# Optimization experiments

Hardware: AMD Instinct MI355X
Metric: run time of the kernel (lower is better)

Reference implementation:

```python
import jax, jax.numpy as jnp
import numpy as np

N_EMB = 1024
N_HEADS = 16
HS = N_EMB // N_HEADS  # 64
BASE = 10000.0


def _rope_cache(T):
    # theta uses dim = n_emb (as in the source), sliced to hs//2 frequencies
    i = jnp.arange(HS // 2, dtype=jnp.float32)
    theta = BASE ** (-2.0 * i / N_EMB)            # [hs/2]
    pos = jnp.arange(T, dtype=jnp.float32)        # [T]
    ang = pos[:, None] * theta[None, :]           # [T, hs/2]
    return jnp.cos(ang), jnp.sin(ang)


def _apply_rope(x, cos, sin):
    # x: [B, T, nh, hs]; rotate consecutive pairs along hs
    b, t, nh, hs = x.shape
    xr = x.reshape(b, t, nh, hs // 2, 2)
    c = cos[None, :, None, :]
    s = sin[None, :, None, :]
    r0 = xr[..., 0] * c - xr[..., 1] * s
    r1 = xr[..., 1] * c + xr[..., 0] * s
    return jnp.stack([r0, r1], axis=-1).reshape(b, t, nh, hs)


def setup_inputs() -> dict:
    key = jax.random.key(0)
    k1, k2, k3, k4 = jax.random.split(key, 4)
    B, T = 2, 2048
    w_std = 0.02
    x = jax.random.normal(k1, (B, T, N_EMB), jnp.float32)
    Wq = jax.random.normal(k2, (N_EMB, N_EMB), jnp.float32) * w_std
    Wk = jax.random.normal(k3, (N_EMB, N_EMB), jnp.float32) * w_std
    Wv = jax.random.normal(k4, (N_EMB, N_EMB), jnp.float32) * w_std
    return {"x": x, "Wq": Wq, "Wk": Wk, "Wv": Wv}


def reference(x, Wq, Wk, Wv):
    B, T, C = x.shape
    # nn.Linear(bias=False): y = x @ W.T
    q = (x @ Wq.T).reshape(B, T, N_HEADS, HS)
    k = (x @ Wk.T).reshape(B, T, N_HEADS, HS)
    v = (x @ Wv.T).reshape(B, T, N_HEADS, HS)
    cos, sin = _rope_cache(T)
    q = _apply_rope(q, cos, sin)
    k = _apply_rope(k, cos, sin)
    # scale uses C (n_emb), as in the source (not head_size)
    wei = jnp.einsum('bqhd,bkhd->bhqk', q, k) * (C ** -0.5)  # [B, nh, T, T]
    mask = jnp.tril(jnp.ones((T, T), dtype=bool))
    wei = jnp.where(mask[None, None], wei, -jnp.inf)
    wei = jax.nn.softmax(wei, axis=-1)
    # dropout is identity in eval mode
    out = jnp.einsum('bhqk,bkhd->bqhd', wei, v).reshape(B, T, C)
    return out
```

## Files before the change

kernel.cpp:

```cpp
#include <hip/hip_runtime.h>
#include <stdint.h>

typedef unsigned short u16;
typedef __bf16 bf16x8 __attribute__((ext_vector_type(8)));
typedef unsigned short u16x8 __attribute__((ext_vector_type(8)));
typedef float f32x4 __attribute__((ext_vector_type(4)));
typedef uint32_t u32v4 __attribute__((ext_vector_type(4)));

#define LOG2E 1.4426950408889634f

typedef const __attribute__((address_space(1))) uint32_t as1_u32;
typedef __attribute__((address_space(3))) uint32_t as3_u32;

__device__ __forceinline__ u16 f2bf(float f) {
  union { float f; uint32_t i; } v; v.f = f;
  uint32_t r = (v.i + 0x7fffu + ((v.i >> 16) & 1u)) >> 16;
  return (u16)r;
}
__device__ __forceinline__ float bf2f(u16 u) {
  union { uint32_t i; float f; } v; v.i = ((uint32_t)u) << 16; return v.f;
}

__device__ __forceinline__ void gld_lds16(const void* g, void* l) {
  as1_u32* gp = (as1_u32*)((uintptr_t)g);
  as3_u32* lp = (as3_u32*)(uint32_t)(uintptr_t)(l);
  __builtin_amdgcn_global_load_lds(gp, lp, 16, 0, 0);
}

__device__ __forceinline__ float fast_exp2(float x) {
  float r;
  asm("v_exp_f32 %0, %1" : "=v"(r) : "v"(x));
  return r;
}

__global__ __launch_bounds__(256) void f32_to_bf16(
    const float* __restrict__ x, const float* __restrict__ wq,
    const float* __restrict__ wk, const float* __restrict__ wv,
    u16* __restrict__ xc, u16* __restrict__ wqc,
    u16* __restrict__ wkc, u16* __restrict__ wvc) {
  const int z = blockIdx.y;
  const float* src = z == 0 ? x : (z == 1 ? wq : (z == 2 ? wk : wv));
  u16* dst = z == 0 ? xc : (z == 1 ? wqc : (z == 2 ? wkc : wvc));
  const int n = z == 0 ? (1 << 22) : (1 << 20);

  const int idx = (blockIdx.x * 256 + (int)threadIdx.x) * 8;
  if (idx >= n) return;
  const f32x4 a = *(const f32x4*)&src[idx];
  const f32x4 b = *(const f32x4*)&src[idx + 4];
  u16x8 o;
#pragma unroll
  for (int j = 0; j < 4; j++) { o[j] = f2bf(a[j]); o[j + 4] = f2bf(b[j]); }
  *(u16x8*)&dst[idx] = o;
}

__global__ __launch_bounds__(256) void qkv_gemm(
    const u16* __restrict__ xc, const u16* __restrict__ wqc,
    const u16* __restrict__ wkc, const u16* __restrict__ wvc,
    u16* __restrict__ qo, u16* __restrict__ ko, u16* __restrict__ vt) {
  __shared__ __align__(16) u16 As[128 * 64];
  __shared__ __align__(16) u16 Bs[128 * 64];

  const int tid = threadIdx.x;
  const int lane = tid & 63;
  const int w = tid >> 6;
  const int wm = w >> 1, wn = w & 1;
  const int quad = lane >> 4, m16 = lane & 15;

  const int id    = (int)blockIdx.x;
  const int xcd   = id & 7;
  const int local = id >> 3;
  const int by    = xcd * 4 + (local & 3);
  const int rest  = local >> 2;
  const int which = rest % 3;
  const int bx    = rest / 3;

  const u16* __restrict__ Ap;
  const u16* __restrict__ Bp;
  int m0, n0;
  if (which == 2) {
    Ap = wvc; Bp = xc;
    m0 = bx * 128;
    n0 = by * 128;
  } else {
    Ap = xc; Bp = which == 0 ? wqc : wkc;
    m0 = by * 128;
    n0 = bx * 128;
  }

  const f32x4 z4 = {0.f, 0.f, 0.f, 0.f};
  f32x4 acc[4][4];
#pragma unroll
  for (int i = 0; i < 4; i++)
#pragma unroll
    for (int j = 0; j < 4; j++) acc[i][j] = z4;

  const int lrow = lane >> 3;
  const int scol = ((lane & 7) ^ (lrow & 7)) * 8;
  const int srowA = m0 + w * 32 + lrow;
  const int srowB = n0 + w * 32 + lrow;
  const int rsw = m16 & 7;

  for (int k0 = 0; k0 < 1024; k0 += 64) {
    __syncthreads();
#pragma unroll
    for (int j = 0; j < 4; j++) {
      gld_lds16(&Ap[(size_t)(srowA + j * 8) * 1024 + k0 + scol],
                &As[(w * 32 + j * 8) * 64]);
      gld_lds16(&Bp[(size_t)(srowB + j * 8) * 1024 + k0 + scol],
                &Bs[(w * 32 + j * 8) * 64]);
    }
    __syncthreads();

#pragma unroll
    for (int kk = 0; kk < 2; kk++) {
      bf16x8 af[4], bfr[4];
#pragma unroll
      for (int t = 0; t < 4; t++) {
        af[t] = *(const bf16x8*)
            &As[(wm * 64 + t * 16 + m16) * 64 + (((kk * 4 + quad) ^ rsw) * 8)];
        bfr[t] = *(const bf16x8*)
            &Bs[(wn * 64 + t * 16 + m16) * 64 + (((kk * 4 + quad) ^ rsw) * 8)];
      }
#pragma unroll
      for (int mt = 0; mt < 4; mt++)
#pragma unroll
        for (int nt = 0; nt < 4; nt++)
          acc[mt][nt] = __builtin_amdgcn_mfma_f32_16x16x32_bf16(
              af[mt], bfr[nt], acc[mt][nt], 0, 0, 0);
    }
  }

  if (which < 2) {
    u16* __restrict__ out = which == 0 ? qo : ko;
#pragma unroll
    for (int mt = 0; mt < 4; mt++) {
      const int row = m0 + wm * 64 + mt * 16 + quad * 4;
#pragma unroll
      for (int nt = 0; nt < 4; nt++) {
        const int n = n0 + wn * 64 + nt * 16 + m16;
        f32x4 a = acc[mt][nt];
#pragma unroll
        for (int r = 0; r < 4; r++)
          out[(size_t)(row + r) * 1024 + n] = f2bf(a[r]);
      }
    }
  } else {
    const int m16p = (m16 & 3) | ((m16 & 4) << 1) | ((m16 & 8) >> 1);
#pragma unroll
    for (int mt = 0; mt < 4; mt++) {
      const int row = m0 + wm * 64 + mt * 16 + quad * 4;
#pragma unroll
      for (int nt = 0; nt < 4; nt++) {
        const int n = n0 + wn * 64 + nt * 16 + m16p;
        f32x4 a = acc[mt][nt];
#pragma unroll
        for (int r = 0; r < 4; r++)
          vt[(size_t)(row + r) * 4096 + n] = f2bf(a[r]);
      }
    }
  }
}

__global__ __launch_bounds__(256) void rope_inplace(u16* __restrict__ qb,
                                                    u16* __restrict__ kb) {
  u16* buf = blockIdx.y == 0 ? qb : kb;
  const int p = blockIdx.x * 256 + (int)threadIdx.x;
  const int e0 = p * 8;
  const int row = e0 >> 10;
  const int col0 = e0 & 1023;
  const int t = row & 2047;
  const float tf = (float)t;

  u16x8 d = *(const u16x8*)&buf[(size_t)row * 1024 + col0];
  u16x8 o;
#pragma unroll
  for (int j = 0; j < 4; j++) {
    const int i = ((col0 & 63) >> 1) + j;
    const float th = fast_exp2(-(float)i * 0.02595256324130752f);
    const float rev = tf * th * 0.15915494309189535f;
    float fr, s, c;
    asm("v_fract_f32 %0, %1" : "=v"(fr) : "v"(rev));
    asm("v_sin_f32 %0, %1" : "=v"(s) : "v"(fr));
    asm("v_cos_f32 %0, %1" : "=v"(c) : "v"(fr));
    const float a0 = bf2f(d[2 * j]), a1 = bf2f(d[2 * j + 1]);
    o[2 * j]     = f2bf(a0 * c - a1 * s);
    o[2 * j + 1] = f2bf(a1 * c + a0 * s);
  }
  *(u16x8*)&buf[(size_t)row * 1024 + col0] = o;
}

__global__ __launch_bounds__(256, 2) void flash_attn(
    const u16* __restrict__ qg, const u16* __restrict__ kg,
    const u16* __restrict__ vt, float* __restrict__ out) {
  __shared__ __align__(16) u16 Ks[2][128 * 72];
  __shared__ __align__(16) u16 Vs[2][64 * 136];

  const int tid = threadIdx.x, lane = tid & 63, w = tid >> 6;
  const int quad = lane >> 4, m16 = lane & 15;

  const int id    = (int)blockIdx.x;
  const int lower = id & 255;
  const int j     = id >> 8;
  const int X     = lower & 7;
  const int vloc  = (lower >> 3) & 3;
  const int kk_   = lower >> 5;
  const int Q     = j ? 15 - kk_ : kk_;
  const int v     = X * 4 + vloc;
  const int h     = v & 15;
  const int b     = v >> 4;

  const size_t base  = (size_t)b * 2048 * 1024 + (size_t)h * 64;
  const size_t vbase = (size_t)(h * 64) * 4096 + (size_t)b * 2048;
  const float SC = 0.03125f * LOG2E;
  const f32x4 z4 = {0.f, 0.f, 0.f, 0.f};
  const int srow = tid >> 2, sc = (tid & 3) * 16;

  union { u16x8 u; bf16x8 f; } ones;
#pragma unroll
  for (int k = 0; k < 8; k++) ones.u[k] = 0x3F80;

  const int q0 = Q * 128;
  const int nr = Q + 1;

  const u16* qsA = &qg[base + (size_t)(q0 + w * 32 + m16) * 1024 + quad * 8];
  const bf16x8 qfA0 = *(const bf16x8*)qsA;
  const bf16x8 qfA1 = *(const bf16x8*)(qsA + 32);
  const u16* qsB = qsA + (size_t)16 * 1024;
  const bf16x8 qfB0 = *(const bf16x8*)qsB;
  const bf16x8 qfB1 = *(const bf16x8*)(qsB + 32);

  u16x8 kr0, kr1, kr2, kr3, vr0, vr1, vr2, vr3;
  {
    const u16* ks = &kg[base + (size_t)srow * 1024 + sc];
    kr0 = *(const u16x8*)ks; kr1 = *(const u16x8*)(ks + 8);
    const u16* ks2 = ks + (size_t)64 * 1024;
    kr2 = *(const u16x8*)ks2; kr3 = *(const u16x8*)(ks2 + 8);
    const u16* vs = &vt[vbase + (size_t)srow * 4096 + sc];
    vr0 = *(const u16x8*)vs; vr1 = *(const u16x8*)(vs + 8);
    vr2 = *(const u16x8*)(vs + 64); vr3 = *(const u16x8*)(vs + 72);
  }

  f32x4 lA = z4, lB = z4;
  f32x4 OA[4], OB[4];
#pragma unroll
  for (int d = 0; d < 4; d++) { OA[d] = z4; OB[d] = z4; }

  const int qrowA = q0 + w * 32 + quad * 4;
  const int qcolA = q0 + w * 32 + m16;

  int p = 0;
  for (int rr = 0; rr < nr; ++rr) {
    const int k0 = rr * 128;
    u16* ksp = &Ks[p][0];
    u16* vsp = &Vs[p][0];
    *(u16x8*)&ksp[srow * 72 + sc] = kr0;
    *(u16x8*)&ksp[srow * 72 + sc + 8] = kr1;
    *(u16x8*)&ksp[(64 + srow) * 72 + sc] = kr2;
    *(u16x8*)&ksp[(64 + srow) * 72 + sc + 8] = kr3;
    *(u16x8*)&vsp[srow * 136 + sc] = vr0;
    *(u16x8*)&vsp[srow * 136 + sc + 8] = vr1;
    *(u16x8*)&vsp[srow * 136 + 64 + sc] = vr2;
    *(u16x8*)&vsp[srow * 136 + 64 + sc + 8] = vr3;
    if (rr + 1 < nr) {
      const u16* ks = &kg[base + (size_t)(k0 + 128 + srow) * 1024 + sc];
      kr0 = *(const u16x8*)ks; kr1 = *(const u16x8*)(ks + 8);
      const u16* ks2 = ks + (size_t)64 * 1024;
      kr2 = *(const u16x8*)ks2; kr3 = *(const u16x8*)(ks2 + 8);
      const u16* vs = &vt[vbase + (size_t)srow * 4096 + k0 + 128 + sc];
      vr0 = *(const u16x8*)vs; vr1 = *(const u16x8*)(vs + 8);
      vr2 = *(const u16x8*)(vs + 64); vr3 = *(const u16x8*)(vs + 72);
    }
    __syncthreads();

    f32x4 SA[8], SB[8];
#pragma unroll
    for (int nt = 0; nt < 8; nt++) {
      const bf16x8 kf0 = *(const bf16x8*)&ksp[(nt * 16 + m16) * 72 + quad * 8];
      const bf16x8 kf1 =
          *(const bf16x8*)&ksp[(nt * 16 + m16) * 72 + 32 + quad * 8];
      SA[nt] = __builtin_amdgcn_mfma_f32_16x16x32_bf16(kf0, qfA0, z4, 0, 0, 0);
      SA[nt] = __builtin_amdgcn_mfma_f32_16x16x32_bf16(kf1, qfA1, SA[nt], 0, 0, 0);
      SB[nt] = __builtin_amdgcn_mfma_f32_16x16x32_bf16(kf0, qfB0, z4, 0, 0, 0);
      SB[nt] = __builtin_amdgcn_mfma_f32_16x16x32_bf16(kf1, qfB1, SB[nt], 0, 0, 0);
    }

    const bool lastr = (rr == nr - 1);

    union { u32v4 u; bf16x8 f; } PA[4], PB[4];
    {
      uint32_t W[16];
#pragma unroll
      for (int nt = 0; nt < 8; nt++) {
        float pe[4];
#pragma unroll
        for (int r = 0; r < 4; r++) {
          float e = fast_exp2(SA[nt][r] * SC);
          const int key = k0 + nt * 16 + quad * 4 + r;
          if (lastr && key > qcolA) e = 0.f;
          pe[r] = e;
        }
        uint32_t w0, w1;
        asm("v_cvt_pk_bf16_f32 %0, %1, %2" : "=v"(w0) : "v"(pe[0]), "v"(pe[1]));
        asm("v_cvt_pk_bf16_f32 %0, %1, %2" : "=v"(w1) : "v"(pe[2]), "v"(pe[3]));
        W[2 * nt] = w0; W[2 * nt + 1] = w1;
      }
#pragma unroll
      for (int ks = 0; ks < 4; ks++) {
        uint32_t a0 = W[4 * ks], b0 = W[4 * ks + 2];
        uint32_t a1 = W[4 * ks + 1], b1 = W[4 * ks + 3];
        asm("v_permlane32_swap_b32 %0, %1" : "+v"(a0), "+v"(b0));
        asm("v_permlane32_swap_b32 %0, %1" : "+v"(a1), "+v"(b1));
        PA[ks].u = (u32v4){a0, a1, b0, b1};
      }
    }
    {
      const int qcolB = qcolA + 16;
      uint32_t W[16];
#pragma unroll
      for (int nt = 0; nt < 8; nt++) {
        float pe[4];
#pragma unroll
        for (int r = 0; r < 4; r++) {
          float e = fast_exp2(SB[nt][r] * SC);
          const int key = k0 + nt * 16 + quad * 4 + r;
          if (lastr && key > qcolB) e = 0.f;
          pe[r] = e;
        }
        uint32_t w0, w1;
        asm("v_cvt_pk_bf16_f32 %0, %1, %2" : "=v"(w0) : "v"(pe[0]), "v"(pe[1]));
        asm("v_cvt_pk_bf16_f32 %0, %1, %2" : "=v"(w1) : "v"(pe[2]), "v"(pe[3]));
        W[2 * nt] = w0; W[2 * nt + 1] = w1;
      }
#pragma unroll
      for (int ks = 0; ks < 4; ks++) {
        uint32_t a0 = W[4 * ks], b0 = W[4 * ks + 2];
        uint32_t a1 = W[4 * ks + 1], b1 = W[4 * ks + 3];
        asm("v_permlane32_swap_b32 %0, %1" : "+v"(a0), "+v"(b0));
        asm("v_permlane32_swap_b32 %0, %1" : "+v"(a1), "+v"(b1));
        PB[ks].u = (u32v4){a0, a1, b0, b1};
      }
    }

#pragma unroll
    for (int ks = 0; ks < 4; ks++) {
      lA = __builtin_amdgcn_mfma_f32_16x16x32_bf16(PA[ks].f, ones.f, lA, 0, 0, 0);
      lB = __builtin_amdgcn_mfma_f32_16x16x32_bf16(PB[ks].f, ones.f, lB, 0, 0, 0);
    }

#pragma unroll
    for (int dt = 0; dt < 4; dt++) {
#pragma unroll
      for (int ks = 0; ks < 4; ks++) {
        const bf16x8 vf =
            *(const bf16x8*)&vsp[(dt * 16 + m16) * 136 + ks * 32 + quad * 8];
        OA[dt] = __builtin_amdgcn_mfma_f32_16x16x32_bf16(PA[ks].f, vf, OA[dt],
                                                         0, 0, 0);
        OB[dt] = __builtin_amdgcn_mfma_f32_16x16x32_bf16(PB[ks].f, vf, OB[dt],
                                                         0, 0, 0);
      }
    }
    p ^= 1;
  }

  float invA[4], invB[4];
#pragma unroll
  for (int r = 0; r < 4; r++) { invA[r] = 1.0f / lA[r]; invB[r] = 1.0f / lB[r]; }

#pragma unroll
  for (int dt = 0; dt < 4; dt++)
#pragma unroll
    for (int r = 0; r < 4; r++) {
      out[base + (size_t)(qrowA + r) * 1024 + dt * 16 + m16] =
          OA[dt][r] * invA[r];
      out[base + (size_t)(qrowA + 16 + r) * 1024 + dt * 16 + m16] =
          OB[dt][r] * invB[r];
    }
}

extern "C" void kernel_launch(void* const* d_in, const int* in_sizes, int n_in,
                              void* d_out, int out_size, void* d_ws, size_t ws_size,
                              hipStream_t stream) {
  const float* x  = (const float*)d_in[0];
  const float* Wq = (const float*)d_in[1];
  const float* Wk = (const float*)d_in[2];
  const float* Wv = (const float*)d_in[3];
  u16* qb  = (u16*)d_ws;
  u16* kb  = qb  + (size_t)4096 * 1024;
  u16* vtw = kb  + (size_t)4096 * 1024;
  u16* xc  = vtw + (size_t)4096 * 1024;
  u16* wqc = xc  + (size_t)4096 * 1024;
  u16* wkc = wqc + (size_t)1024 * 1024;
  u16* wvc = wkc + (size_t)1024 * 1024;

  f32_to_bf16<<<dim3(2048, 4), 256, 0, stream>>>(x, Wq, Wk, Wv,
                                                 xc, wqc, wkc, wvc);
  qkv_gemm<<<dim3(768, 1, 1), 256, 0, stream>>>(xc, wqc, wkc, wvc,
                                                qb, kb, vtw);
  rope_inplace<<<dim3(2048, 2), 256, 0, stream>>>(qb, kb);
  flash_attn<<<dim3(512, 1, 1), 256, 0, stream>>>(qb, kb, vtw, (float*)d_out);
}
```

Measured before the change: 152.7 us.

## Load V fragments directly from global memory instead of staging through LDS

Removes the shared-memory V tile and its register prefetch. Each wave now loads its V^T MFMA operands straight from global memory into registers, issued mid-iteration so they overlap the softmax of the B half. The barrier moves to right after the K tile store, ahead of the next K prefetch. This cuts LDS traffic and footprint but makes every wave fetch V independently from global/L2, with 16 extra live bf16x8 registers and latency exposed inside the loop.

```diff
diff --git a/kernel.cpp b/kernel.cpp
--- a/kernel.cpp
+++ b/kernel.cpp
@@ -193,7 +193,6 @@
     const u16* __restrict__ qg, const u16* __restrict__ kg,
     const u16* __restrict__ vt, float* __restrict__ out) {
   __shared__ __align__(16) u16 Ks[2][128 * 72];
-  __shared__ __align__(16) u16 Vs[2][64 * 136];
 
   const int tid = threadIdx.x, lane = tid & 63, w = tid >> 6;
   const int quad = lane >> 4, m16 = lane & 15;
@@ -229,15 +228,12 @@
   const bf16x8 qfB0 = *(const bf16x8*)qsB;
   const bf16x8 qfB1 = *(const bf16x8*)(qsB + 32);
 
-  u16x8 kr0, kr1, kr2, kr3, vr0, vr1, vr2, vr3;
+  u16x8 kr0, kr1, kr2, kr3;
   {
-    const u16* ks = &kg[base + (size_t)srow * 1024 + sc];
-    kr0 = *(const u16x8*)ks; kr1 = *(const u16x8*)(ks + 8);
-    const u16* ks2 = ks + (size_t)64 * 1024;
-    kr2 = *(const u16x8*)ks2; kr3 = *(const u16x8*)(ks2 + 8);
-    const u16* vs = &vt[vbase + (size_t)srow * 4096 + sc];
-    vr0 = *(const u16x8*)vs; vr1 = *(const u16x8*)(vs + 8);
-    vr2 = *(const u16x8*)(vs + 64); vr3 = *(const u16x8*)(vs + 72);
+    const u16* kp = &kg[base + (size_t)srow * 1024 + sc];
+    kr0 = *(const u16x8*)kp; kr1 = *(const u16x8*)(kp + 8);
+    const u16* kp2 = kp + (size_t)64 * 1024;
+    kr2 = *(const u16x8*)kp2; kr3 = *(const u16x8*)(kp2 + 8);
   }
 
   f32x4 lA = z4, lB = z4;
@@ -252,25 +248,18 @@
   for (int rr = 0; rr < nr; ++rr) {
     const int k0 = rr * 128;
     u16* ksp = &Ks[p][0];
-    u16* vsp = &Vs[p][0];
     *(u16x8*)&ksp[srow * 72 + sc] = kr0;
     *(u16x8*)&ksp[srow * 72 + sc + 8] = kr1;
     *(u16x8*)&ksp[(64 + srow) * 72 + sc] = kr2;
     *(u16x8*)&ksp[(64 + srow) * 72 + sc + 8] = kr3;
-    *(u16x8*)&vsp[srow * 136 + sc] = vr0;
-    *(u16x8*)&vsp[srow * 136 + sc + 8] = vr1;
-    *(u16x8*)&vsp[srow * 136 + 64 + sc] = vr2;
-    *(u16x8*)&vsp[srow * 136 + 64 + sc + 8] = vr3;
+    __syncthreads();
+
     if (rr + 1 < nr) {
-      const u16* ks = &kg[base + (size_t)(k0 + 128 + srow) * 1024 + sc];
-      kr0 = *(const u16x8*)ks; kr1 = *(const u16x8*)(ks + 8);
-      const u16* ks2 = ks + (size_t)64 * 1024;
-      kr2 = *(const u16x8*)ks2; kr3 = *(const u16x8*)(ks2 + 8);
-      const u16* vs = &vt[vbase + (size_t)srow * 4096 + k0 + 128 + sc];
-      vr0 = *(const u16x8*)vs; vr1 = *(const u16x8*)(vs + 8);
-      vr2 = *(const u16x8*)(vs + 64); vr3 = *(const u16x8*)(vs + 72);
-    }
-    __syncthreads();
+      const u16* kp = &kg[base + (size_t)(k0 + 128 + srow) * 1024 + sc];
+      kr0 = *(const u16x8*)kp; kr1 = *(const u16x8*)(kp + 8);
+      const u16* kp2 = kp + (size_t)64 * 1024;
+      kr2 = *(const u16x8*)kp2; kr3 = *(const u16x8*)(kp2 + 8);
+    }
 
     f32x4 SA[8], SB[8];
 #pragma unroll
@@ -313,6 +302,15 @@
         PA[ks].u = (u32v4){a0, a1, b0, b1};
       }
     }
+
+    bf16x8 vf[4][4];
+#pragma unroll
+    for (int dt = 0; dt < 4; dt++)
+#pragma unroll
+      for (int ks = 0; ks < 4; ks++)
+        vf[dt][ks] = *(const bf16x8*)
+            &vt[vbase + (size_t)(dt * 16 + m16) * 4096 + k0 + ks * 32 + quad * 8];
+
     {
       const int qcolB = qcolA + 16;
       uint32_t W[16];
@@ -351,12 +349,10 @@
     for (int dt = 0; dt < 4; dt++) {
 #pragma unroll
       for (int ks = 0; ks < 4; ks++) {
-        const bf16x8 vf =
-            *(const bf16x8*)&vsp[(dt * 16 + m16) * 136 + ks * 32 + quad * 8];
-        OA[dt] = __builtin_amdgcn_mfma_f32_16x16x32_bf16(PA[ks].f, vf, OA[dt],
-                                                         0, 0, 0);
-        OB[dt] = __builtin_amdgcn_mfma_f32_16x16x32_bf16(PB[ks].f, vf, OB[dt],
-                                                         0, 0, 0);
+        OA[dt] = __builtin_amdgcn_mfma_f32_16x16x32_bf16(PA[ks].f, vf[dt][ks],
+                                                         OA[dt], 0, 0, 0);
+        OB[dt] = __builtin_amdgcn_mfma_f32_16x16x32_bf16(PB[ks].f, vf[dt][ks],
+                                                         OB[dt], 0, 0, 0);
       }
     }
     p ^= 1;
```

New measurement: 173.1 us. 13.4% more time.

## Triple-buffer QKV GEMM LDS tiles with async prefetch two stages ahead

Applied to the files above, without the earlier changes.

Replaces the single-buffered 64-wide K loop in the QKV projection GEMM with a three-stage ring of 32-wide LDS tiles, so each iteration issues direct global-to-LDS loads two k-steps ahead. Explicit vmcnt/lgkmcnt waits and a single barrier per step stand in for the double __syncthreads. The swizzle is adapted to the narrower tile. This is meant to hide global load latency behind MFMA work, at the cost of more barriers (32 vs 16 k-steps) and fragile hand-tuned wait counts.

```diff
diff --git a/kernel.cpp b/kernel.cpp
--- a/kernel.cpp
+++ b/kernel.cpp
@@ -57,8 +57,8 @@
     const u16* __restrict__ xc, const u16* __restrict__ wqc,
     const u16* __restrict__ wkc, const u16* __restrict__ wvc,
     u16* __restrict__ qo, u16* __restrict__ ko, u16* __restrict__ vt) {
-  __shared__ __align__(16) u16 As[128 * 64];
-  __shared__ __align__(16) u16 Bs[128 * 64];
+  __shared__ __align__(16) u16 As[3][128 * 32];
+  __shared__ __align__(16) u16 Bs[3][128 * 32];
 
   const int tid = threadIdx.x;
   const int lane = tid & 63;
@@ -94,41 +94,51 @@
 #pragma unroll
     for (int j = 0; j < 4; j++) acc[i][j] = z4;
 
-  const int lrow = lane >> 3;
-  const int scol = ((lane & 7) ^ (lrow & 7)) * 8;
+  const int lrow = lane >> 2;
+  const int scol = ((lane & 3) ^ ((lane >> 3) & 3)) * 8;
   const int srowA = m0 + w * 32 + lrow;
   const int srowB = n0 + w * 32 + lrow;
-  const int rsw = m16 & 7;
-
-  for (int k0 = 0; k0 < 1024; k0 += 64) {
-    __syncthreads();
-#pragma unroll
-    for (int j = 0; j < 4; j++) {
-      gld_lds16(&Ap[(size_t)(srowA + j * 8) * 1024 + k0 + scol],
-                &As[(w * 32 + j * 8) * 64]);
-      gld_lds16(&Bp[(size_t)(srowB + j * 8) * 1024 + k0 + scol],
-                &Bs[(w * 32 + j * 8) * 64]);
-    }
-    __syncthreads();
-
-#pragma unroll
-    for (int kk = 0; kk < 2; kk++) {
-      bf16x8 af[4], bfr[4];
-#pragma unroll
-      for (int t = 0; t < 4; t++) {
-        af[t] = *(const bf16x8*)
-            &As[(wm * 64 + t * 16 + m16) * 64 + (((kk * 4 + quad) ^ rsw) * 8)];
-        bfr[t] = *(const bf16x8*)
-            &Bs[(wn * 64 + t * 16 + m16) * 64 + (((kk * 4 + quad) ^ rsw) * 8)];
-      }
-#pragma unroll
-      for (int mt = 0; mt < 4; mt++)
-#pragma unroll
-        for (int nt = 0; nt < 4; nt++)
-          acc[mt][nt] = __builtin_amdgcn_mfma_f32_16x16x32_bf16(
-              af[mt], bfr[nt], acc[mt][nt], 0, 0, 0);
-    }
-  }
+  const int rchunk = (quad ^ ((m16 >> 1) & 3)) * 8;
+
+#define QKV_STAGE(T, B)                                                      \
+  {                                                                          \
+    const int kk0 = (T) * 32;                                                \
+    _Pragma("unroll")                                                        \
+    for (int j2 = 0; j2 < 2; j2++) {                                         \
+      gld_lds16(&Ap[(size_t)(srowA + j2 * 16) * 1024 + kk0 + scol],          \
+                &As[B][(w * 32 + j2 * 16) * 32]);                            \
+      gld_lds16(&Bp[(size_t)(srowB + j2 * 16) * 1024 + kk0 + scol],          \
+                &Bs[B][(w * 32 + j2 * 16) * 32]);                            \
+    }                                                                        \
+  }
+
+  QKV_STAGE(0, 0);
+  QKV_STAGE(1, 1);
+
+  for (int t = 0; t < 32; t++) {
+    const int b = t % 3;
+    asm volatile("s_waitcnt lgkmcnt(0)" ::: "memory");
+    if (t < 31)
+      asm volatile("s_waitcnt vmcnt(4)" ::: "memory");
+    else
+      asm volatile("s_waitcnt vmcnt(0)" ::: "memory");
+    __builtin_amdgcn_s_barrier();
+    if (t + 2 < 32) QKV_STAGE(t + 2, (t + 2) % 3);
+
+    bf16x8 af[4], bfr[4];
+#pragma unroll
+    for (int tt = 0; tt < 4; tt++) {
+      af[tt]  = *(const bf16x8*)&As[b][(wm * 64 + tt * 16 + m16) * 32 + rchunk];
+      bfr[tt] = *(const bf16x8*)&Bs[b][(wn * 64 + tt * 16 + m16) * 32 + rchunk];
+    }
+#pragma unroll
+    for (int mt = 0; mt < 4; mt++)
+#pragma unroll
+      for (int nt = 0; nt < 4; nt++)
+        acc[mt][nt] = __builtin_amdgcn_mfma_f32_16x16x32_bf16(
+            af[mt], bfr[nt], acc[mt][nt], 0, 0, 0);
+  }
+#undef QKV_STAGE
 
   if (which < 2) {
     u16* __restrict__ out = which == 0 ? qo : ko;
```

Result: slower. 155.7 us (+2.0%).
